# Performance work log

Measured on AMD Instinct MI355X. Metric: run time of the kernel, lower is better.

## Reference

```python
import jax, jax.numpy as jnp
import numpy as np

BN_EPS = 1e-5

def _resize_hw(x, hw):
    # bilinear per temporal slice (align_corners=False == jax half-pixel 'linear');
    # T dim keeps its size so linear resize is identity along it.
    B, C, T, H, W = x.shape
    return jax.image.resize(x, (B, C, T, hw, hw), method='linear')

def setup_inputs() -> dict:
    key = jax.random.key(0)
    ks = jax.random.split(key, 12)
    Cin, Cmid = 80, 40
    s = lambda k, shp, scale=0.05: jax.random.normal(k, shp, dtype=jnp.float32) * scale
    return {
        'fast': jax.random.normal(ks[0], (1, Cin, 4, 64, 64), dtype=jnp.float32),
        'slow': jax.random.normal(ks[1], (1, Cin, 4, 64, 64), dtype=jnp.float32),
        'g_w': s(ks[2], (Cmid, Cin)), 'g_b': s(ks[3], (Cmid,)),
        'th_w': s(ks[4], (Cmid, Cin)), 'th_b': s(ks[5], (Cmid,)),
        'ph_w': s(ks[6], (Cmid, Cin)), 'ph_b': s(ks[7], (Cmid,)),
        'wz_w': s(ks[8], (Cin, Cmid)), 'wz_b': s(ks[9], (Cin,)),
        'bn_g': 1.0 + s(ks[10], (Cin,)), 'bn_b': s(ks[11], (Cin,)),
    }

def reference(fast, slow, g_w, g_b, th_w, th_b, ph_w, ph_b, wz_w, wz_b, bn_g, bn_b):
    x_fast = _resize_hw(fast, 32)   # [B,80,4,32,32]
    x_slow = _resize_hw(slow, 32)
    B, C, T, H, W = x_fast.shape
    N = T * H * W
    flat = x_fast.reshape(B, C, N)                      # [B,C,N]
    # 1x1 conv projections (channel contractions)
    g_x = jnp.einsum('oc,bcn->bno', g_w, flat) + g_b          # [B,N,Cm]
    theta = jnp.einsum('oc,bcn->bno', th_w, flat) + th_b      # [B,N,Cm]
    phi = jnp.einsum('oc,bcn->bon', ph_w, flat) + ph_b[None, :, None]  # [B,Cm,N]
    f = jnp.einsum('bnc,bcm->bnm', theta, phi)          # [B,N,N] full attention scores
    f_div_C = jax.nn.softmax(f, axis=-1)                # 'embedded' mode
    y = jnp.einsum('bnm,bmc->bnc', f_div_C, g_x)        # [B,N,Cm]
    y = y.transpose(0, 2, 1).reshape(B, -1, T, H, W)    # [B,Cm,T,H,W]
    # W_z: 1x1 conv then training-mode BatchNorm3d (batch stats over N,T,H,W)
    wy = jnp.einsum('oc,bcthw->bothw', wz_w, y) + wz_b[None, :, None, None, None]
    mean = jnp.mean(wy, axis=(0, 2, 3, 4), keepdims=True)
    var = jnp.var(wy, axis=(0, 2, 3, 4), keepdims=True)
    gamma = bn_g[None, :, None, None, None]
    beta = bn_b[None, :, None, None, None]
    wy = (wy - mean) * jax.lax.rsqrt(var + BN_EPS) * gamma + beta
    z = wy * x_slow                                     # elementwise fast/slow fusion
    return _resize_hw(z, 64)                            # [B,80,4,64,64]
```

## Files before the change

kernel.cpp:

```cpp
#include <hip/hip_runtime.h>

typedef unsigned int u32;
typedef __bf16 bf16x8 __attribute__((ext_vector_type(8)));
typedef float f32x4 __attribute__((ext_vector_type(4)));
typedef u32 u32x4 __attribute__((ext_vector_type(4)));


static __device__ __forceinline__ u32 f2bf(float f) {
    u32 u = __float_as_uint(f);
    return (u + 0x7fffu + ((u >> 16) & 1u)) >> 16;
}

__device__ __forceinline__ void taps_down(int i, int* j, float* w) {
    if (i == 0) {
        j[0]=0; j[1]=0; j[2]=1; j[3]=2;
        w[0]=0.f; w[1]=3.f/7.f; w[2]=3.f/7.f; w[3]=1.f/7.f;
    } else if (i == 31) {
        j[0]=61; j[1]=62; j[2]=63; j[3]=63;
        w[0]=1.f/7.f; w[1]=3.f/7.f; w[2]=3.f/7.f; w[3]=0.f;
    } else {
        j[0]=2*i-1; j[1]=2*i; j[2]=2*i+1; j[3]=2*i+2;
        w[0]=0.125f; w[1]=0.375f; w[2]=0.375f; w[3]=0.125f;
    }
}

__global__ __launch_bounds__(256) void k_down(
        const float* __restrict__ fast, const float* __restrict__ slow,
        float* __restrict__ xf, float* __restrict__ xs) {
    int idx = blockIdx.x * 256 + threadIdx.x;
    int which = idx >= 327680;
    int rem = which ? idx - 327680 : idx;
    const float* src = which ? slow : fast;
    float* dst = which ? xs : xf;
    int c = rem >> 12;
    int n = rem & 4095;
    int tt = n >> 10, hh = (n >> 5) & 31, ww = n & 31;
    int jy[4], jx[4]; float wy[4], wx[4];
    taps_down(hh, jy, wy);
    taps_down(ww, jx, wx);
    const float* base = src + ((c * 4 + tt) << 12);
    float acc = 0.f;
#pragma unroll
    for (int a = 0; a < 4; ++a) {
        const float* row = base + (jy[a] << 6);
        acc += wy[a] * (wx[0]*row[jx[0]] + wx[1]*row[jx[1]]
                      + wx[2]*row[jx[2]] + wx[3]*row[jx[3]]);
    }
    dst[rem] = acc;
}

__global__ __launch_bounds__(256) void k_proj(
        const float* __restrict__ xf,
        const float* __restrict__ gw, const float* __restrict__ gb,
        const float* __restrict__ thw, const float* __restrict__ thb,
        const float* __restrict__ phw, const float* __restrict__ phb,
        unsigned short* __restrict__ gxP, unsigned short* __restrict__ thetaP,
        unsigned short* __restrict__ phiP) {
    __shared__ float sW[480];
    __shared__ float sB[6];
    int t = threadIdx.x;
    int o0 = blockIdx.y * 2;
    for (int i = t; i < 480; i += 256) {
        int mat = i / 160, rem = i % 160;
        int oo = rem / 80, c = rem % 80;
        const float* w = (mat == 0) ? gw : ((mat == 1) ? thw : phw);
        sW[i] = w[(o0 + oo) * 80 + c];
    }
    if (t < 6) {
        int mat = t / 2, oo = t % 2;
        const float* b = (mat == 0) ? gb : ((mat == 1) ? thb : phb);
        sB[t] = b[o0 + oo];
    }
    __syncthreads();
    int n = blockIdx.x * 256 + t;
    if (blockIdx.y == 0) {
#pragma unroll
        for (int c = 40; c < 64; ++c) { thetaP[n*64 + c] = 0; phiP[n*64 + c] = 0; }
#pragma unroll
        for (int r = 40; r < 48; ++r) gxP[r * 4096 + n] = 0;
    }
    float x[80];
#pragma unroll
    for (int c = 0; c < 80; ++c) x[c] = xf[c * 4096 + n];
#pragma unroll
    for (int mat = 0; mat < 3; ++mat) {
#pragma unroll
        for (int oo = 0; oo < 2; ++oo) {
            float acc = sB[mat * 2 + oo];
            const float4* w4 = (const float4*)&sW[mat * 160 + oo * 80];
#pragma unroll
            for (int cq = 0; cq < 20; ++cq) {
                float4 w = w4[cq];
                acc += w.x * x[cq*4] + w.y * x[cq*4+1] + w.z * x[cq*4+2] + w.w * x[cq*4+3];
            }
            int o = o0 + oo;
            if (mat == 0)      gxP[o * 4096 + n]  = (unsigned short)f2bf(acc);
            else if (mat == 1) thetaP[n * 64 + o] = (unsigned short)f2bf(acc);
            else               phiP[n * 64 + o]   = (unsigned short)f2bf(acc);
        }
    }
}

#define YMM(acc, gfr, bfr) \
    acc = __builtin_amdgcn_mfma_f32_16x16x32_bf16( \
        __builtin_bit_cast(bf16x8, gfr), __builtin_bit_cast(bf16x8, bfr), acc, 0, 0, 0)

__global__ __launch_bounds__(256) void k_attn(
        const unsigned short* __restrict__ thetaP,
        const unsigned short* __restrict__ phiP,
        const unsigned short* __restrict__ gxP,
        float* __restrict__ ypart, float* __restrict__ spart) {
    int lane = threadIdx.x & 63;
    int wv = threadIdx.x >> 6;
    int n0 = blockIdx.x * 64 + wv * 16;
    int ck = blockIdx.y;
    int nl = lane & 15, q = lane >> 4;

    const unsigned short* thp = thetaP + (n0 + nl) * 64 + q * 8;
    u32x4 tb0 = *(const u32x4*)(thp);
    u32x4 tb1 = *(const u32x4*)(thp + 32);

    f32x4 y0 = {0.f,0.f,0.f,0.f}, y1 = y0, y2 = y0;
    float ssum = 0.f;
    int idx0 = ((((q & 1) << 5) + nl) << 2);
    int idx1 = idx0 + 64;

    u32x4 pfA[4], pfB[4], gfA[3], gfB[3];
    int mbase = ck * 512;

#define LOADBLK(P, G, BLK) do {                                              \
        int m0_ = mbase + (BLK) * 32;                                        \
        const unsigned short* pp0_ = phiP + (m0_ + nl) * 64 + q * 8;         \
        const unsigned short* pp1_ = phiP + (m0_ + 16 + nl) * 64 + q * 8;    \
        P[0] = *(const u32x4*)pp0_;  P[1] = *(const u32x4*)(pp0_ + 32);      \
        P[2] = *(const u32x4*)pp1_;  P[3] = *(const u32x4*)(pp1_ + 32);      \
        G[0] = *(const u32x4*)(gxP + (nl) * 4096      + m0_ + q * 8);        \
        G[1] = *(const u32x4*)(gxP + (16 + nl) * 4096 + m0_ + q * 8);        \
        G[2] = *(const u32x4*)(gxP + (32 + nl) * 4096 + m0_ + q * 8);        \
    } while (0)

#define COMPUTE(P, G) do {                                                   \
        u32 p0[2], p1[2];                                                    \
        _Pragma("unroll")                                                    \
        for (int Tm = 0; Tm < 2; ++Tm) {                                     \
            f32x4 f = {0.f,0.f,0.f,0.f};                                     \
            f = __builtin_amdgcn_mfma_f32_16x16x32_bf16(                     \
                __builtin_bit_cast(bf16x8, P[Tm*2+0]),                       \
                __builtin_bit_cast(bf16x8, tb0), f, 0, 0, 0);                \
            f = __builtin_amdgcn_mfma_f32_16x16x32_bf16(                     \
                __builtin_bit_cast(bf16x8, P[Tm*2+1]),                       \
                __builtin_bit_cast(bf16x8, tb1), f, 0, 0, 0);                \
            float e0 = __expf(f[0]), e1 = __expf(f[1]);                      \
            float e2 = __expf(f[2]), e3 = __expf(f[3]);                      \
            ssum += (e0 + e1) + (e2 + e3);                                   \
            p0[Tm] = f2bf(e0) | (f2bf(e1) << 16);                            \
            p1[Tm] = f2bf(e2) | (f2bf(e3) << 16);                            \
        }                                                                    \
        int a0 = __builtin_amdgcn_ds_bpermute(idx0, (int)p0[0]);             \
        int a1 = __builtin_amdgcn_ds_bpermute(idx0, (int)p1[0]);             \
        int a2 = __builtin_amdgcn_ds_bpermute(idx1, (int)p0[0]);             \
        int a3 = __builtin_amdgcn_ds_bpermute(idx1, (int)p1[0]);             \
        int b0 = __builtin_amdgcn_ds_bpermute(idx0, (int)p0[1]);             \
        int b1 = __builtin_amdgcn_ds_bpermute(idx0, (int)p1[1]);             \
        int b2 = __builtin_amdgcn_ds_bpermute(idx1, (int)p0[1]);             \
        int b3 = __builtin_amdgcn_ds_bpermute(idx1, (int)p1[1]);             \
        u32x4 bf_;                                                           \
        bf_[0] = (u32)(q < 2 ? a0 : b0);  bf_[1] = (u32)(q < 2 ? a1 : b1);   \
        bf_[2] = (u32)(q < 2 ? a2 : b2);  bf_[3] = (u32)(q < 2 ? a3 : b3);   \
        YMM(y0, G[0], bf_);  YMM(y1, G[1], bf_);  YMM(y2, G[2], bf_);        \
    } while (0)

    LOADBLK(pfA, gfA, 0);
#pragma unroll 1
    for (int bb = 0; bb < 8; ++bb) {
        LOADBLK(pfB, gfB, bb * 2 + 1);
        COMPUTE(pfA, gfA);
        if (bb < 7) LOADBLK(pfA, gfA, bb * 2 + 2);
        COMPUTE(pfB, gfB);
    }

    ssum += __shfl_xor(ssum, 16);
    ssum += __shfl_xor(ssum, 32);
    if (q == 0) spart[ck * 4096 + n0 + nl] = ssum;

    float* yp = ypart + (size_t)ck * 48 * 4096 + n0 + nl;
#pragma unroll
    for (int r = 0; r < 4; ++r) yp[(q * 4 + r) * 4096] = y0[r];
#pragma unroll
    for (int r = 0; r < 4; ++r) yp[(16 + q * 4 + r) * 4096] = y1[r];
#pragma unroll
    for (int r = 0; r < 4; ++r) yp[(32 + q * 4 + r) * 4096] = y2[r];
}

__global__ __launch_bounds__(256) void k_combine(
        const float* __restrict__ ypart, const float* __restrict__ spart,
        float* __restrict__ yfin) {
    int idx = blockIdx.x * 256 + threadIdx.x;
    int o = idx >> 10;
    int n4 = (idx & 1023) * 4;
    float4 sv[8];
#pragma unroll
    for (int ck = 0; ck < 8; ++ck)
        sv[ck] = *(const float4*)(spart + ck * 4096 + n4);
    float4 yv[8];
#pragma unroll
    for (int ck = 0; ck < 8; ++ck)
        yv[ck] = *(const float4*)(ypart + (size_t)(ck * 48 + o) * 4096 + n4);
    float4 ss = make_float4(0.f,0.f,0.f,0.f), acc = ss;
#pragma unroll
    for (int ck = 0; ck < 8; ++ck) {
        ss.x += sv[ck].x; ss.y += sv[ck].y; ss.z += sv[ck].z; ss.w += sv[ck].w;
        acc.x += yv[ck].x; acc.y += yv[ck].y; acc.z += yv[ck].z; acc.w += yv[ck].w;
    }
    float4 r = make_float4(acc.x/ss.x, acc.y/ss.y, acc.z/ss.z, acc.w/ss.w);
    *(float4*)(yfin + o * 4096 + n4) = r;
}

__device__ __forceinline__ void taps_up(int i, int* j0, int* j1, float* w0, float* w1) {
    if (i == 0)        { *j0 = 0;        *j1 = 0;          *w0 = 0.f;   *w1 = 1.f;   }
    else if (i == 63)  { *j0 = 31;       *j1 = 31;         *w0 = 1.f;   *w1 = 0.f;   }
    else if (i & 1)    { *j0 = i >> 1;   *j1 = (i>>1) + 1; *w0 = 0.75f; *w1 = 0.25f; }
    else               { *j0 = (i>>1)-1; *j1 = i >> 1;     *w0 = 0.25f; *w1 = 0.75f; }
}

__global__ __launch_bounds__(256) void k_bn_up(
        const float* __restrict__ yfin, const float* __restrict__ wzw,
        const float* __restrict__ wzb, const float* __restrict__ bng,
        const float* __restrict__ bnb, const float* __restrict__ xs,
        float* __restrict__ out) {
    __shared__ float4 wrow4[1024];
    __shared__ float sred[8];
    int ch = blockIdx.x;
    int t = threadIdx.x;
    float w[40];
#pragma unroll
    for (int o = 0; o < 40; ++o) w[o] = wzw[ch * 40 + o];
    float bias = wzb[ch];
    float s1 = 0.f, s2 = 0.f;
#pragma unroll 1
    for (int k = 0; k < 4; ++k) {
        int i = k * 256 + t;
        float4 yv[40];
#pragma unroll
        for (int o = 0; o < 40; ++o)
            yv[o] = *(const float4*)(yfin + o * 4096 + i * 4);
        float4 a = make_float4(bias, bias, bias, bias);
#pragma unroll
        for (int o = 0; o < 40; ++o) {
            a.x += w[o]*yv[o].x; a.y += w[o]*yv[o].y;
            a.z += w[o]*yv[o].z; a.w += w[o]*yv[o].w;
        }
        wrow4[i] = a;
        s1 += a.x + a.y + a.z + a.w;
        s2 += a.x*a.x + a.y*a.y + a.z*a.z + a.w*a.w;
    }
#pragma unroll
    for (int off = 32; off > 0; off >>= 1) {
        s1 += __shfl_down(s1, off);
        s2 += __shfl_down(s2, off);
    }
    int wid = t >> 6;
    if ((t & 63) == 0) { sred[wid] = s1; sred[4 + wid] = s2; }
    __syncthreads();
    float mean = (sred[0] + sred[1] + sred[2] + sred[3]) * (1.f / 4096.f);
    float var  = (sred[4] + sred[5] + sred[6] + sred[7]) * (1.f / 4096.f) - mean * mean;
    float inv = rsqrtf(var + 1e-5f);
    float sc = bng[ch] * inv;
    float sh = bnb[ch] - mean * sc;
#pragma unroll
    for (int k = 0; k < 4; ++k) {
        int i = k * 256 + t;
        float4 a = wrow4[i];
        float4 xv = *(const float4*)(xs + ch * 4096 + i * 4);
        a.x = (a.x*sc + sh)*xv.x; a.y = (a.y*sc + sh)*xv.y;
        a.z = (a.z*sc + sh)*xv.z; a.w = (a.w*sc + sh)*xv.w;
        wrow4[i] = a;
    }
    __syncthreads();
    const float* zs = (const float*)wrow4;
    int chbase = ch << 14;
#pragma unroll 4
    for (int k = 0; k < 64; ++k) {
        int p = k * 256 + t;
        int tt = p >> 12, yy = (p >> 6) & 63, xx = p & 63;
        int jy0, jy1, jx0, jx1; float wy0, wy1, wx0, wx1;
        taps_up(yy, &jy0, &jy1, &wy0, &wy1);
        taps_up(xx, &jx0, &jx1, &wx0, &wx1);
        const float* pl = zs + tt * 1024;
        float r0 = wx0*pl[jy0*32 + jx0] + wx1*pl[jy0*32 + jx1];
        float r1 = wx0*pl[jy1*32 + jx0] + wx1*pl[jy1*32 + jx1];
        out[chbase + p] = wy0*r0 + wy1*r1;
    }
}

extern "C" void kernel_launch(void* const* d_in, const int* in_sizes, int n_in,
                              void* d_out, int out_size, void* d_ws, size_t ws_size,
                              hipStream_t stream) {
    const float* fast = (const float*)d_in[0];
    const float* slow = (const float*)d_in[1];
    const float* g_w  = (const float*)d_in[2];
    const float* g_b  = (const float*)d_in[3];
    const float* th_w = (const float*)d_in[4];
    const float* th_b = (const float*)d_in[5];
    const float* ph_w = (const float*)d_in[6];
    const float* ph_b = (const float*)d_in[7];
    const float* wz_w = (const float*)d_in[8];
    const float* wz_b = (const float*)d_in[9];
    const float* bn_g = (const float*)d_in[10];
    const float* bn_b = (const float*)d_in[11];
    float* out = (float*)d_out;
    float* ws  = (float*)d_ws;

    float* xf = ws;
    float* xs = ws + 327680;
    unsigned short* thetaP = (unsigned short*)(ws + 655360);
    unsigned short* phiP   = (unsigned short*)(ws + 786432);
    unsigned short* gxP    = (unsigned short*)(ws + 917504);
    float* ypart = ws + 1015808;
    float* spart = ws + 2588672;
    float* yfin  = ws + 2621440;

    k_down<<<2560, 256, 0, stream>>>(fast, slow, xf, xs);
    k_proj<<<dim3(16, 20), 256, 0, stream>>>(xf, g_w, g_b, th_w, th_b, ph_w, ph_b,
                                             gxP, thetaP, phiP);
    k_attn<<<dim3(64, 8), 256, 0, stream>>>(thetaP, phiP, gxP, ypart, spart);
    k_combine<<<160, 256, 0, stream>>>(ypart, spart, yfin);
    k_bn_up<<<80, 256, 0, stream>>>(yfin, wz_w, wz_b, bn_g, bn_b, xs, out);
}
```

Baseline: 144.5 us.

## Fuse split-K attention combine into attention kernel via shared-memory reduction

Each attention block now handles 16 query rows, with its four waves splitting the key range and reducing partial outputs and softmax sums in shared memory before writing normalized y. This removes the separate combine kernel and the global partial buffers. In exchange, the grid halves to 256 blocks and each wave runs twice as many loop iterations, reducing parallelism and latency hiding.

```diff
diff --git a/kernel.cpp b/kernel.cpp
--- a/kernel.cpp
+++ b/kernel.cpp
@@ -109,11 +109,13 @@
         const unsigned short* __restrict__ thetaP,
         const unsigned short* __restrict__ phiP,
         const unsigned short* __restrict__ gxP,
-        float* __restrict__ ypart, float* __restrict__ spart) {
-    int lane = threadIdx.x & 63;
-    int wv = threadIdx.x >> 6;
-    int n0 = blockIdx.x * 64 + wv * 16;
-    int ck = blockIdx.y;
+        float* __restrict__ yfin) {
+    __shared__ float yred[4][48][16];
+    __shared__ float sred[4][16];
+    int t = threadIdx.x;
+    int lane = t & 63;
+    int wv = t >> 6;
+    int n0 = blockIdx.x * 16;
     int nl = lane & 15, q = lane >> 4;
 
     const unsigned short* thp = thetaP + (n0 + nl) * 64 + q * 8;
@@ -126,7 +128,7 @@
     int idx1 = idx0 + 64;
 
     u32x4 pfA[4], pfB[4], gfA[3], gfB[3];
-    int mbase = ck * 512;
+    int mbase = wv * 1024;
 
 #define LOADBLK(P, G, BLK) do {                                              \
         int m0_ = mbase + (BLK) * 32;                                        \
@@ -172,48 +174,33 @@
 
     LOADBLK(pfA, gfA, 0);
 #pragma unroll 1
-    for (int bb = 0; bb < 8; ++bb) {
+    for (int bb = 0; bb < 16; ++bb) {
         LOADBLK(pfB, gfB, bb * 2 + 1);
         COMPUTE(pfA, gfA);
-        if (bb < 7) LOADBLK(pfA, gfA, bb * 2 + 2);
+        if (bb < 15) LOADBLK(pfA, gfA, bb * 2 + 2);
         COMPUTE(pfB, gfB);
     }
 
     ssum += __shfl_xor(ssum, 16);
     ssum += __shfl_xor(ssum, 32);
-    if (q == 0) spart[ck * 4096 + n0 + nl] = ssum;
-
-    float* yp = ypart + (size_t)ck * 48 * 4096 + n0 + nl;
-#pragma unroll
-    for (int r = 0; r < 4; ++r) yp[(q * 4 + r) * 4096] = y0[r];
-#pragma unroll
-    for (int r = 0; r < 4; ++r) yp[(16 + q * 4 + r) * 4096] = y1[r];
-#pragma unroll
-    for (int r = 0; r < 4; ++r) yp[(32 + q * 4 + r) * 4096] = y2[r];
-}
-
-__global__ __launch_bounds__(256) void k_combine(
-        const float* __restrict__ ypart, const float* __restrict__ spart,
-        float* __restrict__ yfin) {
-    int idx = blockIdx.x * 256 + threadIdx.x;
-    int o = idx >> 10;
-    int n4 = (idx & 1023) * 4;
-    float4 sv[8];
-#pragma unroll
-    for (int ck = 0; ck < 8; ++ck)
-        sv[ck] = *(const float4*)(spart + ck * 4096 + n4);
-    float4 yv[8];
-#pragma unroll
-    for (int ck = 0; ck < 8; ++ck)
-        yv[ck] = *(const float4*)(ypart + (size_t)(ck * 48 + o) * 4096 + n4);
-    float4 ss = make_float4(0.f,0.f,0.f,0.f), acc = ss;
-#pragma unroll
-    for (int ck = 0; ck < 8; ++ck) {
-        ss.x += sv[ck].x; ss.y += sv[ck].y; ss.z += sv[ck].z; ss.w += sv[ck].w;
-        acc.x += yv[ck].x; acc.y += yv[ck].y; acc.z += yv[ck].z; acc.w += yv[ck].w;
-    }
-    float4 r = make_float4(acc.x/ss.x, acc.y/ss.y, acc.z/ss.z, acc.w/ss.w);
-    *(float4*)(yfin + o * 4096 + n4) = r;
+    if (lane < 16) sred[wv][lane] = ssum;
+#pragma unroll
+    for (int r = 0; r < 4; ++r) {
+        yred[wv][q * 4 + r][nl]      = y0[r];
+        yred[wv][16 + q * 4 + r][nl] = y1[r];
+        yred[wv][32 + q * 4 + r][nl] = y2[r];
+    }
+    __syncthreads();
+
+    for (int v = t; v < 768; v += 256) {
+        int c = v >> 4, n = v & 15;
+        if (c < 40) {
+            float s  = (yred[0][c][n] + yred[1][c][n])
+                     + (yred[2][c][n] + yred[3][c][n]);
+            float ss = (sred[0][n] + sred[1][n]) + (sred[2][n] + sred[3][n]);
+            yfin[c * 4096 + n0 + n] = s / ss;
+        }
+    }
 }
 
 __device__ __forceinline__ void taps_up(int i, int* j0, int* j1, float* w0, float* w1) {
@@ -316,14 +303,11 @@
     unsigned short* thetaP = (unsigned short*)(ws + 655360);
     unsigned short* phiP   = (unsigned short*)(ws + 786432);
     unsigned short* gxP    = (unsigned short*)(ws + 917504);
-    float* ypart = ws + 1015808;
-    float* spart = ws + 2588672;
-    float* yfin  = ws + 2621440;
+    float* yfin  = ws + 1015808;
 
     k_down<<<2560, 256, 0, stream>>>(fast, slow, xf, xs);
     k_proj<<<dim3(16, 20), 256, 0, stream>>>(xf, g_w, g_b, th_w, th_b, ph_w, ph_b,
                                              gxP, thetaP, phiP);
-    k_attn<<<dim3(64, 8), 256, 0, stream>>>(thetaP, phiP, gxP, ypart, spart);
-    k_combine<<<160, 256, 0, stream>>>(ypart, spart, yfin);
+    k_attn<<<256, 256, 0, stream>>>(thetaP, phiP, gxP, yfin);
     k_bn_up<<<80, 256, 0, stream>>>(yfin, wz_w, wz_b, bn_g, bn_b, xs, out);
 }
```

After: 140.6 us (median of 2 runs). 1.03x faster.
